# Kernel optimization log

Measured on AMD Instinct MI355X. Metric: run time of the kernel, lower is better.

## Reference

```python
import jax, jax.numpy as jnp
import numpy as np

N = 500
HG = 16
D = 512
STEPS = 16


def _gcn_norm(edge_index, n):
    # PyG GCNConv: add self-loops, symmetric normalization
    src = jnp.concatenate([edge_index[0], jnp.arange(n)])
    dst = jnp.concatenate([edge_index[1], jnp.arange(n)])
    deg = jax.ops.segment_sum(jnp.ones_like(dst, dtype=jnp.float32), dst, num_segments=n)
    dinv = jnp.where(deg > 0, jax.lax.rsqrt(jnp.maximum(deg, 1.0)), 0.0)
    norm = dinv[src] * dinv[dst]
    return src, dst, norm


def _gcn(h, src, dst, norm, W, b):
    # h: (B, N, F) -> (B, N, HG);  out_i = sum_{j->i} norm_ji * (h_j W) + b
    hW = h @ W                              # (B, N, HG)
    t = jnp.swapaxes(hW, 0, 1)              # (N, B, HG)
    msg = t[src] * norm[:, None, None]      # (E', B, HG)
    agg = jax.ops.segment_sum(msg, dst, num_segments=h.shape[1])
    return jnp.swapaxes(agg, 0, 1) + b


def _gru_step(h, xt, Wih, Whh, bih, bhh):
    gi = xt @ Wih.T + bih                    # (B, 3D)
    gh = h @ Whh.T + bhh
    ir, iz, inn = jnp.split(gi, 3, axis=-1)
    hr, hz, hn = jnp.split(gh, 3, axis=-1)
    r = jax.nn.sigmoid(ir + hr)
    z = jax.nn.sigmoid(iz + hz)
    n = jnp.tanh(inn + r * hn)
    return (1.0 - z) * n + z * h


def setup_inputs() -> dict:
    key = jax.random.key(0)
    ks = jax.random.split(key, 16)
    B, T, F = 32, 64, 8
    E = 16000
    s = lambda fan_in: 1.0 / np.sqrt(fan_in)
    u = lambda k, shape, sc: jax.random.uniform(k, shape, jnp.float32, -sc, sc)
    return {
        "x": jax.random.normal(ks[0], (B, T, N, F), jnp.float32),
        "decoder_initial_input": jax.random.normal(ks[1], (B, N, 1), jnp.float32),
        "edge_index": jax.random.randint(ks[2], (2, E), 0, N),
        "gcn_enc_W": u(ks[3], (F, HG), s(F)),
        "gcn_enc_b": jnp.zeros((HG,), jnp.float32),
        "gcn_dec_W": u(ks[4], (1, HG), 1.0),
        "gcn_dec_b": jnp.zeros((HG,), jnp.float32),
        "enc_Wih": u(ks[5], (3 * D, N * HG), s(D)),
        "enc_Whh": u(ks[6], (3 * D, D), s(D)),
        "enc_bih": u(ks[7], (3 * D,), s(D)),
        "enc_bhh": u(ks[8], (3 * D,), s(D)),
        "dec_Wih": u(ks[9], (3 * D, N * HG), s(D)),
        "dec_Whh": u(ks[10], (3 * D, D), s(D)),
        "dec_bih": u(ks[11], (3 * D,), s(D)),
        "dec_bhh": u(ks[12], (3 * D,), s(D)),
        "fc_W": u(ks[13], (N, D), s(D)),
        "fc_b": u(ks[14], (N,), s(D)),
    }


def reference(x, decoder_initial_input, edge_index,
              gcn_enc_W, gcn_enc_b, gcn_dec_W, gcn_dec_b,
              enc_Wih, enc_Whh, enc_bih, enc_bhh,
              dec_Wih, dec_Whh, dec_bih, dec_bhh,
              fc_W, fc_b):
    B, T, n, F = x.shape
    src, dst, norm = _gcn_norm(edge_index, n)

    # ---- encoder: GCN over all (B,T) at once, then GRU scan over T ----
    emb = jax.nn.relu(_gcn(x.reshape(B * T, n, F), src, dst, norm, gcn_enc_W, gcn_enc_b))
    flat = emb.reshape(B, T, n * HG)
    xs = jnp.swapaxes(flat, 0, 1)            # (T, B, N*HG)
    h0 = jnp.zeros((B, D), jnp.float32)

    def enc_body(h, xt):
        return _gru_step(h, xt, enc_Wih, enc_Whh, enc_bih, enc_bhh), None

    hidden, _ = jax.lax.scan(enc_body, h0, xs)

    def dec_body(carry, _):
        h, inp = carry                        # inp: (B, N, 1)
        e = jax.nn.relu(_gcn(inp, src, dst, norm, gcn_dec_W, gcn_dec_b))
        h = _gru_step(h, e.reshape(B, n * HG), dec_Wih, dec_Whh, dec_bih, dec_bhh)
        out = h @ fc_W.T + fc_b               # (B, N)
        return (h, out[:, :, None]), out

    (_, _), outs = jax.lax.scan(dec_body, (hidden, decoder_initial_input), None, length=STEPS)
    return jnp.swapaxes(outs, 0, 1)           # (B, STEPS, N)
```

## Files before the change

### kernel.cpp

```cpp
#include <hip/hip_runtime.h>
#include <stdint.h>

typedef short short8 __attribute__((ext_vector_type(8)));
typedef float f32x4 __attribute__((ext_vector_type(4)));
typedef float f32x16 __attribute__((ext_vector_type(16)));

#define N_NODES 500
#define HGC 16
#define DH 512
#define T_STEPS 64
#define NB 32
#define F_IN 8
#define DSTEPS 16
#define E_EDGES 16000
#define E_TOT 16500
#define NH 8000
#define G3 1536
#define BT 2048
#define DKC 10
#define DNT 48
#define DBLK 480

__device__ __forceinline__ unsigned short f2bf(float x) {
  unsigned int u = __float_as_uint(x);
  u = (u + 0x7fffu + ((u >> 16) & 1u)) >> 16;
  return (unsigned short)u;
}

__device__ __forceinline__ void gl_lds16(const void* g, void* l) {
  __builtin_amdgcn_global_load_lds((const __attribute__((address_space(1))) void*)g,
                                   (__attribute__((address_space(3))) void*)l, 16, 0, 0);
}

__device__ __forceinline__ float sigm(float x) { return 1.f / (1.f + __expf(-x)); }

__global__ void k_deg_init(int* deg) {
  int t = blockIdx.x * blockDim.x + threadIdx.x;
  if (t < N_NODES) deg[t] = 1;
}

__global__ void k_deg_count(const int* __restrict__ ei, int* deg) {
  int t = blockIdx.x * blockDim.x + threadIdx.x;
  if (t < E_EDGES) atomicAdd(&deg[ei[E_EDGES + t]], 1);
}

__global__ void k_scan(const int* __restrict__ deg, float* dinv, int* rowptr, int* cursor) {
  __shared__ int s[512];
  int t = threadIdx.x;
  int v = (t < N_NODES) ? deg[t] : 0;
  s[t] = v;
  __syncthreads();
  for (int off = 1; off < 512; off <<= 1) {
    int add = (t >= off) ? s[t - off] : 0;
    __syncthreads();
    s[t] += add;
    __syncthreads();
  }
  if (t < N_NODES) {
    int excl = s[t] - v;
    rowptr[t] = excl;
    cursor[t] = excl;
    dinv[t] = rsqrtf((float)v);
  }
  if (t == 0) rowptr[N_NODES] = s[511];
}

__global__ void k_scatter(const int* __restrict__ ei, const float* __restrict__ dinv,
                          int* cursor, int* col, float* nrm) {
  int t = blockIdx.x * blockDim.x + threadIdx.x;
  if (t >= E_TOT) return;
  int s_, d_;
  if (t < E_EDGES) { s_ = ei[t]; d_ = ei[E_EDGES + t]; }
  else { s_ = d_ = t - E_EDGES; }
  int pos = atomicAdd(&cursor[d_], 1);
  col[pos] = s_;
  nrm[pos] = dinv[s_] * dinv[d_];
}

__global__ void k_f2bf4(const float* __restrict__ src, unsigned short* __restrict__ dst, int n4) {
  int i = blockIdx.x * blockDim.x + threadIdx.x;
  if (i >= n4) return;
  float4 v = ((const float4*)src)[i];
  ushort4 o;
  o.x = f2bf(v.x); o.y = f2bf(v.y); o.z = f2bf(v.z); o.w = f2bf(v.w);
  ((ushort4*)dst)[i] = o;
}

__global__ __launch_bounds__(256) void k_repack(const float* __restrict__ dWih,
                                                unsigned short* __restrict__ wihDp) {
  int i = blockIdx.x * 256 + threadIdx.x;
  if (i >= DBLK * 50 * 32) return;
  int blob = i / 1600, r = i - blob * 1600;
  int nd = r >> 5, col = r & 31;
  int ntile = blob / DKC, kc = blob - ntile * DKC;
  const float* src = dWih + (size_t)(ntile * 32 + col) * NH + kc * 800 + nd * 16;
  short8 lo, hi;
#pragma unroll
  for (int c = 0; c < 8; ++c) {
    lo[c] = (short)f2bf(src[c]);
    hi[c] = (short)f2bf(src[c + 8]);
  }
  unsigned short* dst = wihDp + (size_t)blob * 25600 + nd * 512 + col * 8;
  *(short8*)dst = lo;
  *(short8*)(dst + 256) = hi;
}

__global__ __launch_bounds__(256) void k_transpose(const float* __restrict__ x,
                                                   unsigned short* __restrict__ xT2) {
  __shared__ float xs[N_NODES * 9];
  int g = blockIdx.x, t = threadIdx.x;
  const float4* xg = (const float4*)(x + (size_t)g * (N_NODES * F_IN));
  for (int i = t; i < N_NODES * 2; i += 256) {
    float4 v = xg[i];
    int n = i >> 1, fh = (i & 1) * 4;
    float* d = &xs[n * 9 + fh];
    d[0] = v.x; d[1] = v.y; d[2] = v.z; d[3] = v.w;
  }
  __syncthreads();
  int f = t >> 5, u = t & 31;
  short8 lo, hi;
#pragma unroll
  for (int j = 0; j < 8; ++j) {
    int n0 = u * 16 + j, n1 = n0 + 8;
    lo[j] = (short)((n0 < N_NODES) ? f2bf(xs[n0 * 9 + f]) : 0);
    hi[j] = (short)((n1 < N_NODES) ? f2bf(xs[n1 * 9 + f]) : 0);
  }
  unsigned short* dst = xT2 + (size_t)(g * 8 + f) * 512 + u * 16;
  *(short8*)dst = lo;
  *(short8*)(dst + 8) = hi;
}

__global__ __launch_bounds__(256) void k_densify(const int* __restrict__ rowptr,
                                                 const int* __restrict__ col,
                                                 const float* __restrict__ nrm,
                                                 unsigned short* __restrict__ AhatD) {
  __shared__ float row[512];
  int n = blockIdx.x, t = threadIdx.x;
  row[t] = 0.f; row[t + 256] = 0.f;
  __syncthreads();
  if (n < N_NODES) {
    int e1 = rowptr[n + 1];
    for (int e = rowptr[n] + t; e < e1; e += 256) atomicAdd(&row[col[e]], nrm[e]);
  }
  __syncthreads();
  AhatD[n * 512 + t] = f2bf(row[t]);
  AhatD[n * 512 + t + 256] = f2bf(row[t + 256]);
}

__global__ __launch_bounds__(256) void k_gemm_agg(const unsigned short* __restrict__ A,
                                                  const unsigned short* __restrict__ B,
                                                  const float* __restrict__ W,
                                                  const float* __restrict__ bias,
                                                  unsigned short* __restrict__ emb) {
  __shared__ float smem[64 * 129];
  __shared__ float Wsm[F_IN * HGC];
  __shared__ float bsm[HGC];
  unsigned short* As = (unsigned short*)smem;
  unsigned short* Bs = As + 4096;
  int t = threadIdx.x;
  if (t < F_IN * HGC) Wsm[t] = W[t];
  if (t < HGC) bsm[t] = bias[t];
  int m0 = blockIdx.x * 128, n0 = blockIdx.y * 128;
  int wave = t >> 6, lane = t & 63;
  int mh = (wave >> 1) * 64, nh = (wave & 1) * 64;
  int lrow = t >> 2, lslot = t & 3;
  f32x4 acc[4][4];
#pragma unroll
  for (int a = 0; a < 4; ++a)
#pragma unroll
    for (int b = 0; b < 4; ++b) acc[a][b] = (f32x4){0.f, 0.f, 0.f, 0.f};
  const unsigned short* ga0 = A + (size_t)(m0 + lrow) * 512 + lslot * 8;
  const unsigned short* ga1 = A + (size_t)(m0 + 64 + lrow) * 512 + lslot * 8;
  const unsigned short* gb0 = B + (size_t)(n0 + lrow) * 512 + lslot * 8;
  const unsigned short* gb1 = B + (size_t)(n0 + 64 + lrow) * 512 + lslot * 8;
  int rl = lane & 15, ks = lane >> 4;
  for (int kt = 0; kt < 16; ++kt) {
    int k0 = kt * 32;
    gl_lds16(ga0 + k0, &As[t * 8]);
    gl_lds16(ga1 + k0, &As[2048 + t * 8]);
    gl_lds16(gb0 + k0, &Bs[t * 8]);
    gl_lds16(gb1 + k0, &Bs[2048 + t * 8]);
    __syncthreads();
    short8 af[4], bfr[4];
#pragma unroll
    for (int mf = 0; mf < 4; ++mf) af[mf] = *(const short8*)&As[(mh + mf * 16 + rl) * 32 + ks * 8];
#pragma unroll
    for (int nf = 0; nf < 4; ++nf) bfr[nf] = *(const short8*)&Bs[(nh + nf * 16 + rl) * 32 + ks * 8];
#pragma unroll
    for (int mf = 0; mf < 4; ++mf)
#pragma unroll
      for (int nf = 0; nf < 4; ++nf)
        acc[mf][nf] = __builtin_amdgcn_mfma_f32_16x16x32_bf16(af[mf], bfr[nf], acc[mf][nf], 0, 0, 0);
    __syncthreads();
  }
  int rg = lane >> 4;
  for (int p = 0; p < 2; ++p) {
    if ((wave >> 1) == p) {
#pragma unroll
      for (int mf = 0; mf < 4; ++mf)
#pragma unroll
        for (int nf = 0; nf < 4; ++nf)
#pragma unroll
          for (int q = 0; q < 4; ++q)
            smem[(mf * 16 + rg * 4 + q) * 129 + nh + nf * 16 + rl] = acc[mf][nf][q];
    }
    __syncthreads();
    int gl = t >> 5, sub = t & 31;
    int g = blockIdx.x * 16 + p * 8 + gl;
#pragma unroll
    for (int j = 0; j < 4; ++j) {
      int nl = sub + 32 * j, ng = n0 + nl;
      if (ng < N_NODES) {
        float v[8];
#pragma unroll
        for (int f = 0; f < 8; ++f) v[f] = smem[(gl * 8 + f) * 129 + nl];
        short8 o0, o1;
#pragma unroll
        for (int c = 0; c < 8; ++c) {
          float s0 = bsm[c], s1 = bsm[c + 8];
#pragma unroll
          for (int f = 0; f < 8; ++f) {
            s0 += v[f] * Wsm[f * 16 + c];
            s1 += v[f] * Wsm[f * 16 + c + 8];
          }
          o0[c] = (short)f2bf(fmaxf(s0, 0.f));
          o1[c] = (short)f2bf(fmaxf(s1, 0.f));
        }
        unsigned short* dst = emb + (size_t)g * NH + ng * 16;
        *(short8*)dst = o0;
        *(short8*)(dst + 8) = o1;
      }
    }
    __syncthreads();
  }
}

__global__ __launch_bounds__(256) void k_gemm_enc(
    const unsigned short* __restrict__ A, const unsigned short* __restrict__ Bm,
    float* __restrict__ giP2) {
  __shared__ unsigned short As[128 * 32];
  __shared__ unsigned short Bs[64 * 32];
  int t = threadIdx.x;
  int m0 = blockIdx.x * 128, n0 = blockIdx.y * 64;
  int wave = t >> 6, lane = t & 63;
  int mh = (wave >> 1) * 64, nh = (wave & 1) * 32;
  int lrow = t >> 2, lslot = t & 3;
  f32x4 acc[4][2];
#pragma unroll
  for (int a = 0; a < 4; ++a)
#pragma unroll
    for (int b = 0; b < 2; ++b) acc[a][b] = (f32x4){0.f, 0.f, 0.f, 0.f};
  const unsigned short* ga0 = A + (size_t)(m0 + lrow) * NH + lslot * 8;
  const unsigned short* ga1 = A + (size_t)(m0 + 64 + lrow) * NH + lslot * 8;
  const unsigned short* gb0 = Bm + (size_t)(n0 + lrow) * NH + lslot * 8;
  int rl = lane & 15, ks = lane >> 4;
  for (int kt = 0; kt < 250; ++kt) {
    int k0 = kt * 32;
    gl_lds16(ga0 + k0, &As[t * 8]);
    gl_lds16(ga1 + k0, &As[2048 + t * 8]);
    gl_lds16(gb0 + k0, &Bs[t * 8]);
    __syncthreads();
    short8 af[4], bfr[2];
#pragma unroll
    for (int mf = 0; mf < 4; ++mf) af[mf] = *(const short8*)&As[(mh + mf * 16 + rl) * 32 + ks * 8];
#pragma unroll
    for (int nf = 0; nf < 2; ++nf) bfr[nf] = *(const short8*)&Bs[(nh + nf * 16 + rl) * 32 + ks * 8];
#pragma unroll
    for (int mf = 0; mf < 4; ++mf)
#pragma unroll
      for (int nf = 0; nf < 2; ++nf)
        acc[mf][nf] = __builtin_amdgcn_mfma_f32_16x16x32_bf16(af[mf], bfr[nf], acc[mf][nf], 0, 0, 0);
    __syncthreads();
  }
  int rg = lane >> 4;
  int gate = n0 >> 9;
#pragma unroll
  for (int mf = 0; mf < 4; ++mf)
#pragma unroll
    for (int nf = 0; nf < 2; ++nf) {
      int n = n0 + nh + nf * 16 + rl;
      int d = n & 511, blk = d >> 5, cc = d & 31;
#pragma unroll
      for (int q = 0; q < 4; ++q) {
        int m = m0 + mh + mf * 16 + rg * 4 + q;
        int s = m & 63, bb = m >> 6;
        giP2[(size_t)(s * 16 + blk) * 3072 + gate * 1024 + bb * 32 + cc] = acc[mf][nf][q];
      }
    }
}

__device__ __forceinline__ void stage_hb(const unsigned short* __restrict__ src,
                                         unsigned short* hb, int t) {
  int bw = t >> 3, i8 = t & 7;
  short8 v[8];
#pragma unroll
  for (int i = 0; i < 8; ++i)
    v[i] = *(const short8*)((const char*)src + bw * 1024 + i8 * 128 + i * 16);
#pragma unroll
  for (int i = 0; i < 8; ++i) {
    int kb = i8 * 128 + i * 16;
    *(short8*)((char*)hb + bw * 1024 + (kb ^ ((bw & 15) << 4))) = v[i];
  }
}

__device__ __forceinline__ void gru_core_g(const unsigned short* __restrict__ whhB,
                                           const unsigned short* hb, float* gh,
                                           int t, int c0) {
  int lane = t & 63, g = t >> 6;
  int b31 = lane & 31, kg = lane >> 5;
  if (g < 3) {
    f32x16 acc;
#pragma unroll
    for (int q = 0; q < 16; ++q) acc[q] = 0.f;
    const unsigned short* brow = whhB + (size_t)(g * 512 + c0 + b31) * 512 + kg * 8;
    int asw = (b31 & 15) << 4;
#pragma unroll 4
    for (int kk = 0; kk < 32; ++kk) {
      int kb = (kk * 32 + kg * 16) ^ asw;
      short8 a = *(const short8*)((const char*)hb + b31 * 1024 + kb);
      short8 b = *(const short8*)(brow + kk * 16);
      acc = __builtin_amdgcn_mfma_f32_32x32x16_bf16(a, b, acc, 0, 0, 0);
    }
#pragma unroll
    for (int q = 0; q < 16; ++q) {
      int br = (q & 3) + 8 * (q >> 2) + 4 * kg;
      gh[g * 1024 + br * 32 + b31] = acc[q];
    }
  }
}

__device__ __forceinline__ void gru_gates(const float* gi, const float* gh,
                                          const float* __restrict__ bih,
                                          const float* __restrict__ bhh,
                                          float* __restrict__ hF,
                                          unsigned short* __restrict__ hb_out,
                                          int t, int c0) {
  for (int i = t; i < 1024; i += 256) {
    int b = i >> 5, cc = i & 31, d = c0 + cc;
    float gr = gi[i] + bih[d];
    float gz = gi[1024 + i] + bih[512 + d];
    float gn = gi[2048 + i] + bih[1024 + d];
    float hr = gh[b * 32 + cc] + bhh[d];
    float hz = gh[1024 + b * 32 + cc] + bhh[512 + d];
    float hn = gh[2048 + b * 32 + cc] + bhh[1024 + d];
    float r = sigm(gr + hr), z = sigm(gz + hz);
    float nn = tanhf(gn + r * hn);
    float hp = hF[b * 512 + d];
    float hnew = (1.f - z) * nn + z * hp;
    hF[b * 512 + d] = hnew;
    hb_out[b * 512 + d] = f2bf(hnew);
  }
}

__global__ __launch_bounds__(256, 1) void k_enc_scan(
    const unsigned short* __restrict__ whhB, const float* __restrict__ giP2,
    const float* __restrict__ bih, const float* __restrict__ bhh,
    float* __restrict__ hF, unsigned short* __restrict__ hbA,
    unsigned short* __restrict__ hbB, int* __restrict__ arr) {
  __shared__ unsigned short hb[32 * 512];
  __shared__ float gh[3 * 1024];
  __shared__ float h32[1024];
  __shared__ float gi_lds[3072];
  int t = threadIdx.x, bid = blockIdx.x;
  int c0 = bid * 32;
  int lane = t & 63, g = t >> 6;
  int b31 = lane & 31, kg = lane >> 5;

  short8 wreg[32];
  if (g < 3) {
    const unsigned short* brow = whhB + (size_t)(g * 512 + c0 + b31) * 512 + kg * 8;
#pragma unroll
    for (int kk = 0; kk < 32; ++kk) wreg[kk] = *(const short8*)(brow + kk * 16);
  }
  for (int i = t; i < 1024; i += 256) h32[i] = 0.f;
  int cc = t & 31, d = c0 + cc;
  float bi_r = bih[d], bi_z = bih[512 + d], bi_n = bih[1024 + d];
  float bh_r = bhh[d], bh_z = bhh[512 + d], bh_n = bhh[1024 + d];
  int asw = (b31 & 15) << 4;
  {
    const float* src0 = giP2 + (size_t)bid * 3072;
#pragma unroll
    for (int i = 0; i < 3; ++i)
      gl_lds16(src0 + i * 1024 + t * 4, &gi_lds[i * 1024 + t * 4]);
  }
  __syncthreads();

  for (int s = 0; s < T_STEPS; ++s) {
    const unsigned short* hbin = (s & 1) ? hbB : hbA;
    unsigned short* hbout = (s & 1) ? hbA : hbB;
    if (s > 0 && t < 64) {
      for (;;) {
        int v = __hip_atomic_load(&arr[t & 15], __ATOMIC_ACQUIRE, __HIP_MEMORY_SCOPE_AGENT);
        if (__all(v >= s)) break;
        __builtin_amdgcn_s_sleep(1);
      }
    }
    __syncthreads();
    stage_hb(hbin, hb, t);
    __syncthreads();
    if (g < 3) {
      f32x16 acc0, acc1;
#pragma unroll
      for (int q = 0; q < 16; ++q) { acc0[q] = 0.f; acc1[q] = 0.f; }
      const char* abase = (const char*)hb + b31 * 1024;
#pragma unroll
      for (int kk = 0; kk < 32; ++kk) {
        int kb = (kk * 32 + kg * 16) ^ asw;
        short8 a = *(const short8*)(abase + kb);
        if (kk & 1) acc1 = __builtin_amdgcn_mfma_f32_32x32x16_bf16(a, wreg[kk], acc1, 0, 0, 0);
        else acc0 = __builtin_amdgcn_mfma_f32_32x32x16_bf16(a, wreg[kk], acc0, 0, 0, 0);
      }
#pragma unroll
      for (int q = 0; q < 16; ++q) {
        int br = (q & 3) + 8 * (q >> 2) + 4 * kg;
        gh[g * 1024 + br * 32 + b31] = acc0[q] + acc1[q];
      }
    }
    __syncthreads();
#pragma unroll
    for (int j = 0; j < 4; ++j) {
      int i = t + 256 * j;
      int b = (t >> 5) + 8 * j;
      float r = sigm(gi_lds[i] + bi_r + gh[i] + bh_r);
      float z = sigm(gi_lds[1024 + i] + bi_z + gh[1024 + i] + bh_z);
      float nn = tanhf(gi_lds[2048 + i] + bi_n + r * (gh[2048 + i] + bh_n));
      float hnew = (1.f - z) * nn + z * h32[i];
      h32[i] = hnew;
      hbout[b * 512 + d] = f2bf(hnew);
    }
    __syncthreads();
    if (g == 3 && s + 1 < T_STEPS) {
      const float* srcn = giP2 + (size_t)((s + 1) * 16 + bid) * 3072;
#pragma unroll
      for (int i = 0; i < 12; ++i)
        gl_lds16(srcn + (i * 64 + lane) * 4, &gi_lds[(i * 64 + lane) * 4]);
    }
    if (t == 0) {
      __threadfence();
      __hip_atomic_store(&arr[bid], s + 1, __ATOMIC_RELEASE, __HIP_MEMORY_SCOPE_AGENT);
    }
  }
#pragma unroll
  for (int j = 0; j < 4; ++j) {
    int i = t + 256 * j;
    int b = (t >> 5) + 8 * j;
    hF[b * 512 + d] = h32[i];
  }
}

__global__ __launch_bounds__(64) void k_dec_gemm(
    const unsigned short* __restrict__ wihDp, const unsigned short* __restrict__ E8,
    float* __restrict__ parts) {
  __shared__ unsigned short wlds[25600];
  int bid = blockIdx.x, t = threadIdx.x;
  int b31 = t & 31, kg = t >> 5;
  int ntile = bid / DKC, kc = bid - ntile * DKC;
  const unsigned short* src = wihDp + (size_t)bid * 25600;
#pragma unroll 10
  for (int i = 0; i < 50; ++i)
    gl_lds16(src + i * 512 + t * 8, (char*)wlds + i * 1024 + t * 16);
  __syncthreads();
  f32x16 acc0, acc1;
#pragma unroll
  for (int q = 0; q < 16; ++q) { acc0[q] = 0.f; acc1[q] = 0.f; }
  const unsigned short* ea = E8 + (size_t)b31 * NH + kc * 800 + kg * 8;
  const char* wb = (const char*)wlds + kg * 512 + b31 * 16;
#pragma unroll 5
  for (int nd = 0; nd < 50; nd += 2) {
    short8 a0 = *(const short8*)(ea + nd * 16);
    short8 b0 = *(const short8*)(wb + (size_t)nd * 1024);
    short8 a1 = *(const short8*)(ea + (nd + 1) * 16);
    short8 b1 = *(const short8*)(wb + (size_t)(nd + 1) * 1024);
    acc0 = __builtin_amdgcn_mfma_f32_32x32x16_bf16(a0, b0, acc0, 0, 0, 0);
    acc1 = __builtin_amdgcn_mfma_f32_32x32x16_bf16(a1, b1, acc1, 0, 0, 0);
  }
  float* pp = parts + (size_t)(kc * DNT + ntile) * 1024 + b31;
#pragma unroll
  for (int q = 0; q < 16; ++q) {
    int br = (q & 3) + 8 * (q >> 2) + 4 * kg;
    pp[br * 32] = acc0[q] + acc1[q];
  }
}

__global__ __launch_bounds__(256) void k_gru_dec(
    const unsigned short* __restrict__ whhB, const float* __restrict__ parts,
    const float* __restrict__ bih, const float* __restrict__ bhh,
    float* hF, const unsigned short* __restrict__ hb_in, unsigned short* __restrict__ hb_out) {
  __shared__ unsigned short hb[32 * 512];
  __shared__ float gh[3 * 32 * 32];
  __shared__ float gi[3 * 32 * 32];
  int t = threadIdx.x;
  int bid = blockIdx.x;
  int c0 = bid * 32;
  stage_hb(hb_in, hb, t);
  for (int i = t; i < 3072; i += 256) {
    int gg = i >> 10, r = i & 1023, bb = r >> 5, cc2 = r & 31;
    float a = 0.f;
#pragma unroll
    for (int kc = 0; kc < DKC; ++kc)
      a += parts[((size_t)kc * DNT + gg * 16 + bid) * 1024 + bb * 32 + cc2];
    gi[i] = a;
  }
  __syncthreads();
  gru_core_g(whhB, hb, gh, t, c0);
  __syncthreads();
  gru_gates(gi, gh, bih, bhh, hF, hb_out, t, c0);
}

__global__ __launch_bounds__(256) void k_fc_agg(
    const float* __restrict__ hF, const float* __restrict__ fcW, const float* __restrict__ fcb,
    const float* __restrict__ Wd, const float* __restrict__ bd,
    const int* __restrict__ rowptr, const int* __restrict__ col, const float* __restrict__ nrm,
    float* __restrict__ out, unsigned short* __restrict__ E8, int s) {
  __shared__ float hrow[512];
  __shared__ float orow[N_NODES];
  __shared__ float wds[HGC], bds[HGC];
  int b = blockIdx.x, t = threadIdx.x;
  hrow[t] = hF[b * 512 + t];
  hrow[t + 256] = hF[b * 512 + t + 256];
  if (t < HGC) { wds[t] = Wd[t]; bds[t] = bd[t]; }
  __syncthreads();
  for (int n = t; n < N_NODES; n += 256) {
    const float4* wr = (const float4*)(fcW + (size_t)n * DH);
    float a = 0.f;
#pragma unroll 4
    for (int k = 0; k < 128; ++k) {
      float4 wv = wr[k];
      const float4 hv = *(const float4*)&hrow[k * 4];
      a += wv.x * hv.x + wv.y * hv.y + wv.z * hv.z + wv.w * hv.w;
    }
    float o = a + fcb[n];
    orow[n] = o;
    out[(size_t)b * (DSTEPS * N_NODES) + s * N_NODES + n] = o;
  }
  __syncthreads();
  for (int n = t; n < N_NODES; n += 256) {
    int e1 = rowptr[n + 1];
    float a = 0.f;
    for (int e = rowptr[n]; e < e1; ++e) a += nrm[e] * orow[col[e]];
    short8 lo, hi;
#pragma unroll
    for (int c = 0; c < 8; ++c) {
      lo[c] = (short)f2bf(fmaxf(a * wds[c] + bds[c], 0.f));
      hi[c] = (short)f2bf(fmaxf(a * wds[c + 8] + bds[c + 8], 0.f));
    }
    unsigned short* dst = E8 + (size_t)b * NH + n * 16;
    *(short8*)dst = lo;
    *(short8*)(dst + 8) = hi;
  }
}

__global__ __launch_bounds__(256) void k_agg0(
    const float* __restrict__ dec0, const float* __restrict__ Wd, const float* __restrict__ bd,
    const int* __restrict__ rowptr, const int* __restrict__ col, const float* __restrict__ nrm,
    unsigned short* __restrict__ E8) {
  __shared__ float irow[N_NODES];
  __shared__ float wds[HGC], bds[HGC];
  int b = blockIdx.x, t = threadIdx.x;
  for (int n = t; n < N_NODES; n += 256) irow[n] = dec0[b * N_NODES + n];
  if (t < HGC) { wds[t] = Wd[t]; bds[t] = bd[t]; }
  __syncthreads();
  for (int n = t; n < N_NODES; n += 256) {
    int e1 = rowptr[n + 1];
    float a = 0.f;
    for (int e = rowptr[n]; e < e1; ++e) a += nrm[e] * irow[col[e]];
    short8 lo, hi;
#pragma unroll
    for (int c = 0; c < 8; ++c) {
      lo[c] = (short)f2bf(fmaxf(a * wds[c] + bds[c], 0.f));
      hi[c] = (short)f2bf(fmaxf(a * wds[c + 8] + bds[c + 8], 0.f));
    }
    unsigned short* dst = E8 + (size_t)b * NH + n * 16;
    *(short8*)dst = lo;
    *(short8*)(dst + 8) = hi;
  }
}

extern "C" void kernel_launch(void* const* d_in, const int* in_sizes, int n_in,
                              void* d_out, int out_size, void* d_ws, size_t ws_size,
                              hipStream_t stream) {
  const float* x = (const float*)d_in[0];
  const float* dec0 = (const float*)d_in[1];
  const int* ei = (const int*)d_in[2];
  const float* gWe = (const float*)d_in[3];
  const float* gbe = (const float*)d_in[4];
  const float* gWd = (const float*)d_in[5];
  const float* gbd = (const float*)d_in[6];
  const float* eWih = (const float*)d_in[7];
  const float* eWhh = (const float*)d_in[8];
  const float* ebih = (const float*)d_in[9];
  const float* ebhh = (const float*)d_in[10];
  const float* dWih = (const float*)d_in[11];
  const float* dWhh = (const float*)d_in[12];
  const float* dbih = (const float*)d_in[13];
  const float* dbhh = (const float*)d_in[14];
  const float* fcW = (const float*)d_in[15];
  const float* fcb = (const float*)d_in[16];
  float* out = (float*)d_out;
  (void)in_sizes; (void)n_in; (void)out_size; (void)ws_size;

  char* w = (char*)d_ws;
  size_t off = 0;
  auto alloc = [&](size_t bytes) -> void* {
    void* p = w + off;
    off = (off + bytes + 255) & ~(size_t)255;
    return p;
  };
  int* deg = (int*)alloc(512 * 4);
  float* dinv = (float*)alloc(512 * 4);
  int* rowptr = (int*)alloc(512 * 4);
  int* cursor = (int*)alloc(512 * 4);
  int* colA = (int*)alloc(E_TOT * 4);
  float* nrmA = (float*)alloc(E_TOT * 4);
  unsigned short* whhE = (unsigned short*)alloc((size_t)G3 * DH * 2);
  unsigned short* whhD = (unsigned short*)alloc((size_t)G3 * DH * 2);
  unsigned short* AhatD = (unsigned short*)alloc(512 * 512 * 2);
  float* hF = (float*)alloc(NB * DH * 4);
  unsigned short* hbX = (unsigned short*)alloc(NB * DH * 2);
  int* arr = (int*)alloc(256);
  unsigned short* hbY = (unsigned short*)alloc(NB * DH * 2);
  unsigned short* E8 = (unsigned short*)alloc((size_t)NB * NH * 2);
  unsigned short* emb = (unsigned short*)alloc((size_t)BT * NH * 2);
  char* wihE_parts = (char*)alloc((size_t)G3 * NH * 2);
  unsigned short* wihE = (unsigned short*)wihE_parts;
  float* parts = (float*)wihE_parts;
  unsigned short* wihDp = (unsigned short*)alloc((size_t)DBLK * 25600 * 2);
  char* xT2_giP = (char*)alloc((size_t)16384 * 512 * 2);
  unsigned short* xT2 = (unsigned short*)xT2_giP;
  float* giP2 = (float*)xT2_giP;

  hipMemsetAsync(hF, 0, NB * DH * 4 + NB * DH * 2 + 256, stream);

  k_deg_init<<<2, 256, 0, stream>>>(deg);
  k_deg_count<<<(E_EDGES + 255) / 256, 256, 0, stream>>>(ei, deg);
  k_scan<<<1, 512, 0, stream>>>(deg, dinv, rowptr, cursor);
  k_scatter<<<(E_TOT + 255) / 256, 256, 0, stream>>>(ei, dinv, cursor, colA, nrmA);

  int n4w = G3 * NH / 4;
  int n4h = G3 * DH / 4;
  k_f2bf4<<<(n4w + 255) / 256, 256, 0, stream>>>(eWih, wihE, n4w);
  k_f2bf4<<<(n4h + 255) / 256, 256, 0, stream>>>(eWhh, whhE, n4h);
  k_f2bf4<<<(n4h + 255) / 256, 256, 0, stream>>>(dWhh, whhD, n4h);
  k_repack<<<3000, 256, 0, stream>>>(dWih, wihDp);

  k_transpose<<<BT, 256, 0, stream>>>(x, xT2);
  k_densify<<<512, 256, 0, stream>>>(rowptr, colA, nrmA, AhatD);
  k_gemm_agg<<<dim3(128, 4), 256, 0, stream>>>(xT2, AhatD, gWe, gbe, emb);

  k_gemm_enc<<<dim3(BT / 128, G3 / 64), 256, 0, stream>>>(emb, wihE, giP2);

  k_enc_scan<<<16, 256, 0, stream>>>(whhE, giP2, ebih, ebhh, hF, hbX, hbY, arr);

  k_agg0<<<NB, 256, 0, stream>>>(dec0, gWd, gbd, rowptr, colA, nrmA, E8);

  for (int s = 0; s < DSTEPS; ++s) {
    const unsigned short* hbin = (s & 1) ? hbY : hbX;
    unsigned short* hbout = (s & 1) ? hbX : hbY;
    k_dec_gemm<<<DBLK, 64, 0, stream>>>(wihDp, E8, parts);
    k_gru_dec<<<16, 256, 0, stream>>>(whhD, parts, dbih, dbhh, hF, hbin, hbout);
    k_fc_agg<<<NB, 256, 0, stream>>>(hF, fcW, fcb, gWd, gbd, rowptr, colA, nrmA, out, E8, s);
  }
}
```

Before: 1.820 ms.

## Fuse decoder step kernels with flag sync, merge graph prep and casts, widen encoder GEMM tile

The three per-step decoder kernels (input GEMM, GRU, FC plus aggregation) become one kernel whose blocks hand off through global release/acquire flags instead of kernel boundaries. The graph preprocessing kernels are merged into a single block that works in LDS, and the three bf16 casts run as one launch. The encoder input GEMM tile grows from 128x64 to 128x128. The flag spin-waits assume every block of the 480-block grid can be resident at once, which risks deadlock or stalls if they cannot be. Only one wave per block does the MFMA work, so occupancy and latency hiding change.

```diff
diff --git a/kernel.cpp b/kernel.cpp
--- a/kernel.cpp
+++ b/kernel.cpp
@@ -34,56 +34,66 @@
 
 __device__ __forceinline__ float sigm(float x) { return 1.f / (1.f + __expf(-x)); }
 
-__global__ void k_deg_init(int* deg) {
-  int t = blockIdx.x * blockDim.x + threadIdx.x;
-  if (t < N_NODES) deg[t] = 1;
-}
-
-__global__ void k_deg_count(const int* __restrict__ ei, int* deg) {
-  int t = blockIdx.x * blockDim.x + threadIdx.x;
-  if (t < E_EDGES) atomicAdd(&deg[ei[E_EDGES + t]], 1);
-}
-
-__global__ void k_scan(const int* __restrict__ deg, float* dinv, int* rowptr, int* cursor) {
-  __shared__ int s[512];
+__global__ __launch_bounds__(512) void k_graph(const int* __restrict__ ei,
+                                               int* __restrict__ rowptr,
+                                               int* __restrict__ colg, float* __restrict__ nrmg) {
+  __shared__ int degL[512];
+  __shared__ int scanL[512];
+  __shared__ int curL[512];
+  __shared__ float dinvL[512];
   int t = threadIdx.x;
-  int v = (t < N_NODES) ? deg[t] : 0;
-  s[t] = v;
+  degL[t] = (t < N_NODES) ? 1 : 0;
+  __syncthreads();
+  for (int e = t; e < E_EDGES; e += 512) atomicAdd(&degL[ei[E_EDGES + e]], 1);
+  __syncthreads();
+  int v = degL[t];
+  scanL[t] = v;
   __syncthreads();
   for (int off = 1; off < 512; off <<= 1) {
-    int add = (t >= off) ? s[t - off] : 0;
-    __syncthreads();
-    s[t] += add;
-    __syncthreads();
-  }
+    int add = (t >= off) ? scanL[t - off] : 0;
+    __syncthreads();
+    scanL[t] += add;
+    __syncthreads();
+  }
+  int excl = scanL[t] - v;
   if (t < N_NODES) {
-    int excl = s[t] - v;
     rowptr[t] = excl;
-    cursor[t] = excl;
-    dinv[t] = rsqrtf((float)v);
-  }
-  if (t == 0) rowptr[N_NODES] = s[511];
-}
-
-__global__ void k_scatter(const int* __restrict__ ei, const float* __restrict__ dinv,
-                          int* cursor, int* col, float* nrm) {
-  int t = blockIdx.x * blockDim.x + threadIdx.x;
-  if (t >= E_TOT) return;
-  int s_, d_;
-  if (t < E_EDGES) { s_ = ei[t]; d_ = ei[E_EDGES + t]; }
-  else { s_ = d_ = t - E_EDGES; }
-  int pos = atomicAdd(&cursor[d_], 1);
-  col[pos] = s_;
-  nrm[pos] = dinv[s_] * dinv[d_];
-}
-
-__global__ void k_f2bf4(const float* __restrict__ src, unsigned short* __restrict__ dst, int n4) {
+    curL[t] = excl;
+    dinvL[t] = rsqrtf((float)v);
+  }
+  if (t == 0) rowptr[N_NODES] = scanL[511];
+  __syncthreads();
+  for (int e = t; e < E_TOT; e += 512) {
+    int s_, d_;
+    if (e < E_EDGES) { s_ = ei[e]; d_ = ei[E_EDGES + e]; }
+    else { s_ = d_ = e - E_EDGES; }
+    int pos = atomicAdd(&curL[d_], 1);
+    colg[pos] = s_;
+    nrmg[pos] = dinvL[s_] * dinvL[d_];
+  }
+}
+
+__global__ void k_f2bf_all(const float* __restrict__ a, unsigned short* __restrict__ da, int n4a,
+                           const float* __restrict__ b, unsigned short* __restrict__ db, int n4b,
+                           const float* __restrict__ c, unsigned short* __restrict__ dc, int n4c) {
   int i = blockIdx.x * blockDim.x + threadIdx.x;
-  if (i >= n4) return;
-  float4 v = ((const float4*)src)[i];
+  const float* s;
+  unsigned short* d;
+  int j = i;
+  if (j < n4a) { s = a; d = da; }
+  else {
+    j -= n4a;
+    if (j < n4b) { s = b; d = db; }
+    else {
+      j -= n4b;
+      if (j >= n4c) return;
+      s = c; d = dc;
+    }
+  }
+  float4 v = ((const float4*)s)[j];
   ushort4 o;
   o.x = f2bf(v.x); o.y = f2bf(v.y); o.z = f2bf(v.z); o.w = f2bf(v.w);
-  ((ushort4*)dst)[i] = o;
+  ((ushort4*)d)[j] = o;
 }
 
 __global__ __launch_bounds__(256) void k_repack(const float* __restrict__ dWih,
@@ -239,36 +249,38 @@
     const unsigned short* __restrict__ A, const unsigned short* __restrict__ Bm,
     float* __restrict__ giP2) {
   __shared__ unsigned short As[128 * 32];
-  __shared__ unsigned short Bs[64 * 32];
+  __shared__ unsigned short Bs[128 * 32];
   int t = threadIdx.x;
-  int m0 = blockIdx.x * 128, n0 = blockIdx.y * 64;
+  int m0 = blockIdx.x * 128, n0 = blockIdx.y * 128;
   int wave = t >> 6, lane = t & 63;
-  int mh = (wave >> 1) * 64, nh = (wave & 1) * 32;
+  int mh = (wave >> 1) * 64, nh = (wave & 1) * 64;
   int lrow = t >> 2, lslot = t & 3;
-  f32x4 acc[4][2];
+  f32x4 acc[4][4];
 #pragma unroll
   for (int a = 0; a < 4; ++a)
 #pragma unroll
-    for (int b = 0; b < 2; ++b) acc[a][b] = (f32x4){0.f, 0.f, 0.f, 0.f};
+    for (int b = 0; b < 4; ++b) acc[a][b] = (f32x4){0.f, 0.f, 0.f, 0.f};
   const unsigned short* ga0 = A + (size_t)(m0 + lrow) * NH + lslot * 8;
   const unsigned short* ga1 = A + (size_t)(m0 + 64 + lrow) * NH + lslot * 8;
   const unsigned short* gb0 = Bm + (size_t)(n0 + lrow) * NH + lslot * 8;
+  const unsigned short* gb1 = Bm + (size_t)(n0 + 64 + lrow) * NH + lslot * 8;
   int rl = lane & 15, ks = lane >> 4;
   for (int kt = 0; kt < 250; ++kt) {
     int k0 = kt * 32;
     gl_lds16(ga0 + k0, &As[t * 8]);
     gl_lds16(ga1 + k0, &As[2048 + t * 8]);
     gl_lds16(gb0 + k0, &Bs[t * 8]);
-    __syncthreads();
-    short8 af[4], bfr[2];
+    gl_lds16(gb1 + k0, &Bs[2048 + t * 8]);
+    __syncthreads();
+    short8 af[4], bfr[4];
 #pragma unroll
     for (int mf = 0; mf < 4; ++mf) af[mf] = *(const short8*)&As[(mh + mf * 16 + rl) * 32 + ks * 8];
 #pragma unroll
-    for (int nf = 0; nf < 2; ++nf) bfr[nf] = *(const short8*)&Bs[(nh + nf * 16 + rl) * 32 + ks * 8];
+    for (int nf = 0; nf < 4; ++nf) bfr[nf] = *(const short8*)&Bs[(nh + nf * 16 + rl) * 32 + ks * 8];
 #pragma unroll
     for (int mf = 0; mf < 4; ++mf)
 #pragma unroll
-      for (int nf = 0; nf < 2; ++nf)
+      for (int nf = 0; nf < 4; ++nf)
         acc[mf][nf] = __builtin_amdgcn_mfma_f32_16x16x32_bf16(af[mf], bfr[nf], acc[mf][nf], 0, 0, 0);
     __syncthreads();
   }
@@ -277,7 +289,7 @@
 #pragma unroll
   for (int mf = 0; mf < 4; ++mf)
 #pragma unroll
-    for (int nf = 0; nf < 2; ++nf) {
+    for (int nf = 0; nf < 4; ++nf) {
       int n = n0 + nh + nf * 16 + rl;
       int d = n & 511, blk = d >> 5, cc = d & 31;
 #pragma unroll
@@ -448,105 +460,145 @@
   }
 }
 
-__global__ __launch_bounds__(64) void k_dec_gemm(
-    const unsigned short* __restrict__ wihDp, const unsigned short* __restrict__ E8,
-    float* __restrict__ parts) {
-  __shared__ unsigned short wlds[25600];
+__global__ __launch_bounds__(256, 1) void k_dec_step(
+    const unsigned short* __restrict__ wihDp, const unsigned short* __restrict__ whhB,
+    const float* __restrict__ bih, const float* __restrict__ bhh,
+    const float* __restrict__ fcW, const float* __restrict__ fcb,
+    const float* __restrict__ Wd, const float* __restrict__ bd,
+    const int* __restrict__ rowptr, const int* __restrict__ colA, const float* __restrict__ nrmA,
+    unsigned short* __restrict__ E8, float* __restrict__ parts,
+    float* __restrict__ hF, const unsigned short* __restrict__ hb_in,
+    unsigned short* __restrict__ hb_out, float* __restrict__ out,
+    int* __restrict__ fP1, int* __restrict__ fGRU, int s) {
+  __shared__ __align__(16) char smem[57344];
   int bid = blockIdx.x, t = threadIdx.x;
-  int b31 = t & 31, kg = t >> 5;
-  int ntile = bid / DKC, kc = bid - ntile * DKC;
-  const unsigned short* src = wihDp + (size_t)bid * 25600;
-#pragma unroll 10
-  for (int i = 0; i < 50; ++i)
-    gl_lds16(src + i * 512 + t * 8, (char*)wlds + i * 1024 + t * 16);
-  __syncthreads();
-  f32x16 acc0, acc1;
-#pragma unroll
-  for (int q = 0; q < 16; ++q) { acc0[q] = 0.f; acc1[q] = 0.f; }
-  const unsigned short* ea = E8 + (size_t)b31 * NH + kc * 800 + kg * 8;
-  const char* wb = (const char*)wlds + kg * 512 + b31 * 16;
+  int w = t >> 6, lane = t & 63;
+  int b31 = lane & 31, kg = lane >> 5;
+
+  {
+    unsigned short* wlds = (unsigned short*)smem;
+    int ntile = bid / DKC, kc = bid - ntile * DKC;
+    const unsigned short* src = wihDp + (size_t)bid * 25600;
+    for (int i = w; i < 50; i += 4)
+      gl_lds16(src + i * 512 + lane * 8, (char*)wlds + i * 1024 + lane * 16);
+    __syncthreads();
+    if (w == 0) {
+      f32x16 acc0, acc1;
+#pragma unroll
+      for (int q = 0; q < 16; ++q) { acc0[q] = 0.f; acc1[q] = 0.f; }
+      const unsigned short* ea = E8 + (size_t)b31 * NH + kc * 800 + kg * 8;
+      const char* wb = (const char*)wlds + kg * 512 + b31 * 16;
 #pragma unroll 5
-  for (int nd = 0; nd < 50; nd += 2) {
-    short8 a0 = *(const short8*)(ea + nd * 16);
-    short8 b0 = *(const short8*)(wb + (size_t)nd * 1024);
-    short8 a1 = *(const short8*)(ea + (nd + 1) * 16);
-    short8 b1 = *(const short8*)(wb + (size_t)(nd + 1) * 1024);
-    acc0 = __builtin_amdgcn_mfma_f32_32x32x16_bf16(a0, b0, acc0, 0, 0, 0);
-    acc1 = __builtin_amdgcn_mfma_f32_32x32x16_bf16(a1, b1, acc1, 0, 0, 0);
-  }
-  float* pp = parts + (size_t)(kc * DNT + ntile) * 1024 + b31;
-#pragma unroll
-  for (int q = 0; q < 16; ++q) {
-    int br = (q & 3) + 8 * (q >> 2) + 4 * kg;
-    pp[br * 32] = acc0[q] + acc1[q];
-  }
-}
-
-__global__ __launch_bounds__(256) void k_gru_dec(
-    const unsigned short* __restrict__ whhB, const float* __restrict__ parts,
-    const float* __restrict__ bih, const float* __restrict__ bhh,
-    float* hF, const unsigned short* __restrict__ hb_in, unsigned short* __restrict__ hb_out) {
-  __shared__ unsigned short hb[32 * 512];
-  __shared__ float gh[3 * 32 * 32];
-  __shared__ float gi[3 * 32 * 32];
-  int t = threadIdx.x;
-  int bid = blockIdx.x;
-  int c0 = bid * 32;
-  stage_hb(hb_in, hb, t);
-  for (int i = t; i < 3072; i += 256) {
-    int gg = i >> 10, r = i & 1023, bb = r >> 5, cc2 = r & 31;
-    float a = 0.f;
-#pragma unroll
-    for (int kc = 0; kc < DKC; ++kc)
-      a += parts[((size_t)kc * DNT + gg * 16 + bid) * 1024 + bb * 32 + cc2];
-    gi[i] = a;
-  }
-  __syncthreads();
-  gru_core_g(whhB, hb, gh, t, c0);
-  __syncthreads();
-  gru_gates(gi, gh, bih, bhh, hF, hb_out, t, c0);
-}
-
-__global__ __launch_bounds__(256) void k_fc_agg(
-    const float* __restrict__ hF, const float* __restrict__ fcW, const float* __restrict__ fcb,
-    const float* __restrict__ Wd, const float* __restrict__ bd,
-    const int* __restrict__ rowptr, const int* __restrict__ col, const float* __restrict__ nrm,
-    float* __restrict__ out, unsigned short* __restrict__ E8, int s) {
-  __shared__ float hrow[512];
-  __shared__ float orow[N_NODES];
-  __shared__ float wds[HGC], bds[HGC];
-  int b = blockIdx.x, t = threadIdx.x;
-  hrow[t] = hF[b * 512 + t];
-  hrow[t + 256] = hF[b * 512 + t + 256];
-  if (t < HGC) { wds[t] = Wd[t]; bds[t] = bd[t]; }
-  __syncthreads();
-  for (int n = t; n < N_NODES; n += 256) {
-    const float4* wr = (const float4*)(fcW + (size_t)n * DH);
-    float a = 0.f;
+      for (int nd = 0; nd < 50; nd += 2) {
+        short8 a0 = *(const short8*)(ea + nd * 16);
+        short8 b0 = *(const short8*)(wb + (size_t)nd * 1024);
+        short8 a1 = *(const short8*)(ea + (nd + 1) * 16);
+        short8 b1 = *(const short8*)(wb + (size_t)(nd + 1) * 1024);
+        acc0 = __builtin_amdgcn_mfma_f32_32x32x16_bf16(a0, b0, acc0, 0, 0, 0);
+        acc1 = __builtin_amdgcn_mfma_f32_32x32x16_bf16(a1, b1, acc1, 0, 0, 0);
+      }
+      float* pp = parts + (size_t)(kc * DNT + ntile) * 1024 + b31;
+#pragma unroll
+      for (int q = 0; q < 16; ++q) {
+        int br = (q & 3) + 8 * (q >> 2) + 4 * kg;
+        pp[br * 32] = acc0[q] + acc1[q];
+      }
+    }
+    __syncthreads();
+    if (t == 0) {
+      __threadfence();
+      __hip_atomic_store(&fP1[bid], s + 1, __ATOMIC_RELEASE, __HIP_MEMORY_SCOPE_AGENT);
+    }
+  }
+  if (bid >= NB) return;
+
+  if (bid < 16) {
+    if (t < 64) {
+      for (;;) {
+        bool ok = true;
+#pragma unroll
+        for (int i = 0; i < 8; ++i) {
+          int idx = t + (i << 6);
+          if (idx < DBLK)
+            ok &= (__hip_atomic_load(&fP1[idx], __ATOMIC_RELAXED, __HIP_MEMORY_SCOPE_AGENT) >= s + 1);
+        }
+        if (__all(ok)) break;
+        __builtin_amdgcn_s_sleep(2);
+      }
+      __threadfence();
+    }
+    __syncthreads();
+    unsigned short* hb = (unsigned short*)smem;
+    float* gh = (float*)(smem + 32768);
+    float* gi = (float*)(smem + 45056);
+    int c0 = bid * 32;
+    stage_hb(hb_in, hb, t);
+    for (int i = t; i < 3072; i += 256) {
+      int gg = i >> 10, r = i & 1023, bb = r >> 5, cc2 = r & 31;
+      float a = 0.f;
+#pragma unroll
+      for (int kc2 = 0; kc2 < DKC; ++kc2)
+        a += parts[((size_t)kc2 * DNT + gg * 16 + bid) * 1024 + bb * 32 + cc2];
+      gi[i] = a;
+    }
+    __syncthreads();
+    gru_core_g(whhB, hb, gh, t, c0);
+    __syncthreads();
+    gru_gates(gi, gh, bih, bhh, hF, hb_out, t, c0);
+    __syncthreads();
+    if (t == 0) {
+      __threadfence();
+      __hip_atomic_store(&fGRU[bid], s + 1, __ATOMIC_RELEASE, __HIP_MEMORY_SCOPE_AGENT);
+    }
+  }
+
+  {
+    if (t < 64) {
+      for (;;) {
+        int f = __hip_atomic_load(&fGRU[t & 15], __ATOMIC_RELAXED, __HIP_MEMORY_SCOPE_AGENT);
+        if (__all(f >= s + 1)) break;
+        __builtin_amdgcn_s_sleep(1);
+      }
+      __threadfence();
+    }
+    __syncthreads();
+    float* hrow = (float*)smem;
+    float* orow = (float*)(smem + 2048);
+    float* wds = (float*)(smem + 4352);
+    float* bds = (float*)(smem + 4480);
+    int b = bid;
+    hrow[t] = hF[b * 512 + t];
+    if (t < 256) hrow[t + 256] = hF[b * 512 + t + 256];
+    if (t < HGC) { wds[t] = Wd[t]; bds[t] = bd[t]; }
+    __syncthreads();
+    for (int n = t; n < N_NODES; n += 256) {
+      const float4* wr = (const float4*)(fcW + (size_t)n * DH);
+      float a = 0.f;
 #pragma unroll 4
-    for (int k = 0; k < 128; ++k) {
-      float4 wv = wr[k];
-      const float4 hv = *(const float4*)&hrow[k * 4];
-      a += wv.x * hv.x + wv.y * hv.y + wv.z * hv.z + wv.w * hv.w;
-    }
-    float o = a + fcb[n];
-    orow[n] = o;
-    out[(size_t)b * (DSTEPS * N_NODES) + s * N_NODES + n] = o;
-  }
-  __syncthreads();
-  for (int n = t; n < N_NODES; n += 256) {
-    int e1 = rowptr[n + 1];
-    float a = 0.f;
-    for (int e = rowptr[n]; e < e1; ++e) a += nrm[e] * orow[col[e]];
-    short8 lo, hi;
-#pragma unroll
-    for (int c = 0; c < 8; ++c) {
-      lo[c] = (short)f2bf(fmaxf(a * wds[c] + bds[c], 0.f));
-      hi[c] = (short)f2bf(fmaxf(a * wds[c + 8] + bds[c + 8], 0.f));
-    }
-    unsigned short* dst = E8 + (size_t)b * NH + n * 16;
-    *(short8*)dst = lo;
-    *(short8*)(dst + 8) = hi;
+      for (int k = 0; k < 128; ++k) {
+        float4 wv = wr[k];
+        const float4 hv = *(const float4*)&hrow[k * 4];
+        a += wv.x * hv.x + wv.y * hv.y + wv.z * hv.z + wv.w * hv.w;
+      }
+      float o = a + fcb[n];
+      orow[n] = o;
+      out[(size_t)b * (DSTEPS * N_NODES) + s * N_NODES + n] = o;
+    }
+    __syncthreads();
+    for (int n = t; n < N_NODES; n += 256) {
+      int e1 = rowptr[n + 1];
+      float a = 0.f;
+      for (int e = rowptr[n]; e < e1; ++e) a += nrmA[e] * orow[colA[e]];
+      short8 lo, hi;
+#pragma unroll
+      for (int c = 0; c < 8; ++c) {
+        lo[c] = (short)f2bf(fmaxf(a * wds[c] + bds[c], 0.f));
+        hi[c] = (short)f2bf(fmaxf(a * wds[c + 8] + bds[c + 8], 0.f));
+      }
+      unsigned short* dst = E8 + (size_t)b * NH + n * 16;
+      *(short8*)dst = lo;
+      *(short8*)(dst + 8) = hi;
+    }
   }
 }
 
@@ -606,10 +658,7 @@
     off = (off + bytes + 255) & ~(size_t)255;
     return p;
   };
-  int* deg = (int*)alloc(512 * 4);
-  float* dinv = (float*)alloc(512 * 4);
   int* rowptr = (int*)alloc(512 * 4);
-  int* cursor = (int*)alloc(512 * 4);
   int* colA = (int*)alloc(E_TOT * 4);
   float* nrmA = (float*)alloc(E_TOT * 4);
   unsigned short* whhE = (unsigned short*)alloc((size_t)G3 * DH * 2);
@@ -618,6 +667,8 @@
   float* hF = (float*)alloc(NB * DH * 4);
   unsigned short* hbX = (unsigned short*)alloc(NB * DH * 2);
   int* arr = (int*)alloc(256);
+  int* fP1 = (int*)alloc(DBLK * 4);
+  int* fGRU = (int*)alloc(256);
   unsigned short* hbY = (unsigned short*)alloc(NB * DH * 2);
   unsigned short* E8 = (unsigned short*)alloc((size_t)NB * NH * 2);
   unsigned short* emb = (unsigned short*)alloc((size_t)BT * NH * 2);
@@ -629,25 +680,21 @@
   unsigned short* xT2 = (unsigned short*)xT2_giP;
   float* giP2 = (float*)xT2_giP;
 
-  hipMemsetAsync(hF, 0, NB * DH * 4 + NB * DH * 2 + 256, stream);
-
-  k_deg_init<<<2, 256, 0, stream>>>(deg);
-  k_deg_count<<<(E_EDGES + 255) / 256, 256, 0, stream>>>(ei, deg);
-  k_scan<<<1, 512, 0, stream>>>(deg, dinv, rowptr, cursor);
-  k_scatter<<<(E_TOT + 255) / 256, 256, 0, stream>>>(ei, dinv, cursor, colA, nrmA);
+  hipMemsetAsync(hF, 0, NB * DH * 4 + NB * DH * 2 + 256 + DBLK * 4 + 256 + 512, stream);
+
+  k_graph<<<1, 512, 0, stream>>>(ei, rowptr, colA, nrmA);
 
   int n4w = G3 * NH / 4;
   int n4h = G3 * DH / 4;
-  k_f2bf4<<<(n4w + 255) / 256, 256, 0, stream>>>(eWih, wihE, n4w);
-  k_f2bf4<<<(n4h + 255) / 256, 256, 0, stream>>>(eWhh, whhE, n4h);
-  k_f2bf4<<<(n4h + 255) / 256, 256, 0, stream>>>(dWhh, whhD, n4h);
+  k_f2bf_all<<<(n4w + 2 * n4h + 255) / 256, 256, 0, stream>>>(
+      eWih, wihE, n4w, eWhh, whhE, n4h, dWhh, whhD, n4h);
   k_repack<<<3000, 256, 0, stream>>>(dWih, wihDp);
 
   k_transpose<<<BT, 256, 0, stream>>>(x, xT2);
   k_densify<<<512, 256, 0, stream>>>(rowptr, colA, nrmA, AhatD);
   k_gemm_agg<<<dim3(128, 4), 256, 0, stream>>>(xT2, AhatD, gWe, gbe, emb);
 
-  k_gemm_enc<<<dim3(BT / 128, G3 / 64), 256, 0, stream>>>(emb, wihE, giP2);
+  k_gemm_enc<<<dim3(BT / 128, G3 / 128), 256, 0, stream>>>(emb, wihE, giP2);
 
   k_enc_scan<<<16, 256, 0, stream>>>(whhE, giP2, ebih, ebhh, hF, hbX, hbY, arr);
 
@@ -656,8 +703,8 @@
   for (int s = 0; s < DSTEPS; ++s) {
     const unsigned short* hbin = (s & 1) ? hbY : hbX;
     unsigned short* hbout = (s & 1) ? hbX : hbY;
-    k_dec_gemm<<<DBLK, 64, 0, stream>>>(wihDp, E8, parts);
-    k_gru_dec<<<16, 256, 0, stream>>>(whhD, parts, dbih, dbhh, hF, hbin, hbout);
-    k_fc_agg<<<NB, 256, 0, stream>>>(hF, fcW, fcb, gWd, gbd, rowptr, colA, nrmA, out, E8, s);
-  }
-}
+    k_dec_step<<<DBLK, 256, 0, stream>>>(wihDp, whhD, dbih, dbhh, fcW, fcb, gWd, gbd,
+                                         rowptr, colA, nrmA, E8, parts, hF, hbin, hbout,
+                                         out, fP1, fGRU, s);
+  }
+}
```

Result: slower. 2.170 ms (+19.3%).
